# Kernel tuning notes

Measured on AMD Instinct MI355X. Metric: run time of the kernel, lower is better.

Reference implementation:

```python
import jax, jax.numpy as jnp
import numpy as np
from jax import lax

# Mamba hyperparams (mamba_ssm defaults for d_model=768)
D_MODEL = 768
N_LAYER = 8
D_INNER = 2 * D_MODEL          # 1536
D_STATE = 16
DT_RANK = D_MODEL // 16        # 48
D_CONV = 4
BATCH = 4
SEQLEN = 1024


def _ln(x, w, b):
    mu = jnp.mean(x, axis=-1, keepdims=True)
    var = jnp.mean(jnp.square(x - mu), axis=-1, keepdims=True)
    return (x - mu) * lax.rsqrt(var + 1e-5) * w + b


def _silu(x):
    return x * jax.nn.sigmoid(x)


def _mamba_mixer(h, in_proj, conv_w, conv_b, x_proj, dt_w, dt_b, A_log, Dv, out_proj):
    # h: [B, L, d_model]
    xz = jnp.einsum('bld,ed->ble', h, in_proj)          # [B, L, 2*d_inner]
    xm, z = jnp.split(xz, 2, axis=-1)
    # causal depthwise conv1d over time
    xc = lax.conv_general_dilated(
        xm.transpose(0, 2, 1), conv_w, (1,), [(D_CONV - 1, 0)],
        feature_group_count=D_INNER)                    # [B, d_inner, L]
    u = _silu((xc + conv_b[None, :, None]).transpose(0, 2, 1))  # [B, L, d_inner]
    dbc = jnp.einsum('bld,ed->ble', u, x_proj)          # [B, L, dt_rank+2*d_state]
    dt = jax.nn.softplus(jnp.einsum('blr,dr->bld', dbc[..., :DT_RANK], dt_w) + dt_b)
    Bm = dbc[..., DT_RANK:DT_RANK + D_STATE]            # [B, L, d_state]
    Cm = dbc[..., DT_RANK + D_STATE:]                   # [B, L, d_state]
    A = -jnp.exp(A_log)                                 # [d_inner, d_state]

    def step(hstate, inp):
        dt_t, B_t, u_t, C_t = inp                       # [B,d_inner],[B,d_state],[B,d_inner],[B,d_state]
        dA = jnp.exp(dt_t[..., None] * A)               # [B, d_inner, d_state]
        hstate = dA * hstate + (dt_t * u_t)[..., None] * B_t[:, None, :]
        y = jnp.einsum('bds,bs->bd', hstate, C_t)
        return hstate, y

    h0 = jnp.zeros((h.shape[0], D_INNER, D_STATE), h.dtype)
    _, ys = lax.scan(step, h0, (dt.transpose(1, 0, 2), Bm.transpose(1, 0, 2),
                                u.transpose(1, 0, 2), Cm.transpose(1, 0, 2)))
    y = ys.transpose(1, 0, 2) + u * Dv                  # skip connection D*u
    y = y * _silu(z)
    return jnp.einsum('ble,de->bld', y, out_proj)


def setup_inputs() -> dict:
    key = jax.random.key(0)
    ks = jax.random.split(key, 16)
    f32 = jnp.float32
    d = {
        'x': jax.random.normal(ks[0], (BATCH, SEQLEN, D_MODEL), f32),
        'pos': jax.random.normal(ks[1], (BATCH, SEQLEN, D_MODEL), f32),
        'norm_w': jnp.ones((N_LAYER, D_MODEL), f32),
        'norm_b': jnp.zeros((N_LAYER, D_MODEL), f32),
        'in_proj': jax.random.normal(ks[2], (N_LAYER, 2 * D_INNER, D_MODEL), f32) * 0.02,
        'conv_w': jax.random.normal(ks[3], (N_LAYER, D_INNER, 1, D_CONV), f32) * 0.2,
        'conv_b': jnp.zeros((N_LAYER, D_INNER), f32),
        'x_proj': jax.random.normal(ks[4], (N_LAYER, DT_RANK + 2 * D_STATE, D_INNER), f32) * 0.02,
        'dt_w': jax.random.normal(ks[5], (N_LAYER, D_INNER, DT_RANK), f32) * 0.1,
        'dt_b': jax.random.uniform(ks[6], (N_LAYER, D_INNER), f32, -4.0, -2.0),
        'A_log': jnp.broadcast_to(jnp.log(jnp.arange(1, D_STATE + 1, dtype=f32)),
                                  (N_LAYER, D_INNER, D_STATE)).copy(),
        'Dv': jnp.ones((N_LAYER, D_INNER), f32),
        'out_proj': jax.random.normal(ks[7], (N_LAYER, D_MODEL, D_INNER), f32) * 0.02,
        'normf_w': jnp.ones((D_MODEL,), f32),
        'normf_b': jnp.zeros((D_MODEL,), f32),
        'dec_w': jnp.ones((D_MODEL,), f32),
        'dec_b': jnp.zeros((D_MODEL,), f32),
        'return_token_num': 256,
    }
    return d


def reference(x, pos, norm_w, norm_b, in_proj, conv_w, conv_b, x_proj, dt_w, dt_b,
              A_log, Dv, out_proj, normf_w, normf_b, dec_w, dec_b, return_token_num):
    hidden = x + pos
    residual = None
    for l in range(N_LAYER):
        residual = hidden if residual is None else hidden + residual
        h = _ln(residual, norm_w[l], norm_b[l])
        hidden = _mamba_mixer(h, in_proj[l], conv_w[l], conv_b[l], x_proj[l],
                              dt_w[l], dt_b[l], A_log[l], Dv[l], out_proj[l])
    residual = hidden + residual
    hidden = _ln(residual, normf_w, normf_b)
    return _ln(hidden[:, -return_token_num:], dec_w, dec_b)
```

## Files before the change

### kernel.cpp

```cpp
#include <hip/hip_runtime.h>
#include <math.h>

#define D_MODEL 768
#define N_LAYER 8
#define D_INNER 1536
#define D_STATE 16
#define DT_RANK 48
#define D_CONV  4
#define BATCH   4
#define SEQLEN  1024
#define NTOK    (BATCH*SEQLEN)
#define DBC_W   (DT_RANK + 2*D_STATE)
#define NC      64
#define CHUNK_T (SEQLEN/NC)
#define XP_KS   16
#define XP_KSL  (D_INNER/XP_KS)
#define CONV_TCH 16
#define OP_KS   4

typedef __attribute__((ext_vector_type(8))) short short8v;
typedef __attribute__((ext_vector_type(4))) float float4v;

__device__ __forceinline__ void split_bf16(float x, short& hi, short& lo) {
  unsigned u = __float_as_uint(x);
  unsigned r = (u + 0x7fffu + ((u >> 16) & 1u)) >> 16;
  hi = (short)r;
  float fhi = __uint_as_float(r << 16);
  float xl = x - fhi;
  unsigned u2 = __float_as_uint(xl);
  unsigned r2 = (u2 + 0x7fffu + ((u2 >> 16) & 1u)) >> 16;
  lo = (short)r2;
}

__device__ __forceinline__ void gload16(const short* g, short* l) {
  __builtin_amdgcn_global_load_lds(
      (const __attribute__((address_space(1))) void*)g,
      (__attribute__((address_space(3))) void*)l, 16, 0, 0);
}

__global__ __launch_bounds__(256) void split_kernel(
    const float* __restrict__ src, short* __restrict__ hi,
    short* __restrict__ lo, int n4) {
  int stride = gridDim.x * 256;
  for (int i = blockIdx.x * 256 + threadIdx.x; i < n4; i += stride) {
    float4 v = ((const float4*)src)[i];
    short4 h, g;
    split_bf16(v.x, h.x, g.x);
    split_bf16(v.y, h.y, g.y);
    split_bf16(v.z, h.z, g.z);
    split_bf16(v.w, h.w, g.w);
    ((short4*)hi)[i] = h;
    ((short4*)lo)[i] = g;
  }
}

__global__ __launch_bounds__(256) void ln_kernel(
    const float* __restrict__ x, const float* __restrict__ pos,
    float* __restrict__ resid, const float* __restrict__ hy,
    short* __restrict__ hh_hi, short* __restrict__ hh_lo,
    const float* __restrict__ w, const float* __restrict__ b, int first) {
  int row = blockIdx.x;
  int tid = threadIdx.x;
  int base = row * D_MODEL;
  __shared__ float red[256];
  __shared__ float s_mu, s_rs;
  float v[3];
#pragma unroll
  for (int i = 0; i < 3; ++i) {
    int c = tid + i * 256;
    float r;
    if (first) r = x[base + c] + pos[base + c];
    else       r = resid[base + c] + hy[base + c];
    resid[base + c] = r;
    v[i] = r;
  }
  float s = v[0] + v[1] + v[2];
  red[tid] = s; __syncthreads();
  for (int off = 128; off > 0; off >>= 1) {
    if (tid < off) red[tid] += red[tid + off];
    __syncthreads();
  }
  if (tid == 0) s_mu = red[0] / D_MODEL;
  __syncthreads();
  float mu = s_mu;
  float q = 0.f;
#pragma unroll
  for (int i = 0; i < 3; ++i) { float d = v[i] - mu; q += d * d; }
  __syncthreads();
  red[tid] = q; __syncthreads();
  for (int off = 128; off > 0; off >>= 1) {
    if (tid < off) red[tid] += red[tid + off];
    __syncthreads();
  }
  if (tid == 0) s_rs = rsqrtf(red[0] / D_MODEL + 1e-5f);
  __syncthreads();
  float rs = s_rs;
#pragma unroll
  for (int i = 0; i < 3; ++i) {
    int c = tid + i * 256;
    float val = (v[i] - mu) * rs * w[c] + b[c];
    short hv, lv; split_bf16(val, hv, lv);
    hh_hi[base + c] = hv;
    hh_lo[base + c] = lv;
  }
}

__global__ __launch_bounds__(256) void gemm_bf16x3(
    const short* __restrict__ Ahi, const short* __restrict__ Alo, int lda,
    const short* __restrict__ Bhi, const short* __restrict__ Blo, int ldb,
    float* __restrict__ C, int M, int N, int K) {
  const int BK = 32;
  __shared__ short Ash[128][32];
  __shared__ short Asl[128][32];
  __shared__ short Bsh[128][32];
  __shared__ short Bsl[128][32];
  int brow = blockIdx.y * 128;
  int bcol = blockIdx.x * 128;
  int ksl = K / gridDim.z;
  int kbeg = blockIdx.z * ksl;
  int kend = kbeg + ksl;
  float* Cw = C + (size_t)blockIdx.z * M * N;
  int tid = threadIdx.x;
  int wv = tid >> 6, l = tid & 63;
  int wr = (wv >> 1) * 64;
  int wc = (wv & 1) * 64;
  int lrow = l & 15;
  int rslot = ((l >> 4) ^ ((l >> 1) & 3)) * 8;
  int lr = l >> 2;
  int lp = l & 3;
  float4v zero = {0.f, 0.f, 0.f, 0.f};
  float4v acc[4][4];
#pragma unroll
  for (int m = 0; m < 4; ++m)
#pragma unroll
    for (int n = 0; n < 4; ++n) acc[m][n] = zero;

  for (int k0 = kbeg; k0 < kend; k0 += BK) {
#pragma unroll
    for (int half = 0; half < 2; ++half) {
      int row = wv * 32 + half * 16 + lr;
      int s = lp ^ ((row >> 1) & 3);
      int ldsrow = wv * 32 + half * 16;
      size_t ao = (size_t)(brow + row) * lda + k0 + s * 8;
      size_t bo = (size_t)(bcol + row) * ldb + k0 + s * 8;
      gload16(Ahi + ao, &Ash[ldsrow][0]);
      gload16(Alo + ao, &Asl[ldsrow][0]);
      gload16(Bhi + bo, &Bsh[ldsrow][0]);
      gload16(Blo + bo, &Bsl[ldsrow][0]);
    }
    __syncthreads();
    short8v ah[4], al[4];
#pragma unroll
    for (int m = 0; m < 4; ++m) {
      int R = wr + m * 16 + lrow;
      ah[m] = *(const short8v*)&Ash[R][rslot];
      al[m] = *(const short8v*)&Asl[R][rslot];
    }
#pragma unroll
    for (int n = 0; n < 4; ++n) {
      int R = wc + n * 16 + lrow;
      short8v bh = *(const short8v*)&Bsh[R][rslot];
      short8v bl = *(const short8v*)&Bsl[R][rslot];
#pragma unroll
      for (int m = 0; m < 4; ++m) {
        acc[m][n] = __builtin_amdgcn_mfma_f32_16x16x32_bf16(ah[m], bh, acc[m][n], 0, 0, 0);
        acc[m][n] = __builtin_amdgcn_mfma_f32_16x16x32_bf16(ah[m], bl, acc[m][n], 0, 0, 0);
        acc[m][n] = __builtin_amdgcn_mfma_f32_16x16x32_bf16(al[m], bh, acc[m][n], 0, 0, 0);
      }
    }
    __syncthreads();
  }
  int drow = (l >> 4) * 4, dcol = l & 15;
#pragma unroll
  for (int m = 0; m < 4; ++m)
#pragma unroll
    for (int n = 0; n < 4; ++n)
#pragma unroll
      for (int j = 0; j < 4; ++j)
        Cw[(size_t)(brow + wr + m * 16 + drow + j) * N + bcol + wc + n * 16 + dcol] =
            acc[m][n][j];
}

__global__ __launch_bounds__(256) void reduce_out_kernel(
    const float* __restrict__ part, float* __restrict__ out, int n4) {
  int i = blockIdx.x * 256 + threadIdx.x;
  if (i >= n4) return;
  float4 s = ((const float4*)part)[i];
#pragma unroll
  for (int k = 1; k < OP_KS; ++k) {
    float4 v = ((const float4*)(part + (size_t)k * NTOK * D_MODEL))[i];
    s.x += v.x; s.y += v.y; s.z += v.z; s.w += v.w;
  }
  ((float4*)out)[i] = s;
}

__global__ __launch_bounds__(256) void gemm_abt(
    const float* __restrict__ A, int lda, const float* __restrict__ B, int ldb,
    float* __restrict__ C, int M, int N, int K) {
  const int BM = 128, BN = 128, BK = 16;
  __shared__ __align__(16) float As[BK][BM + 4];
  __shared__ __align__(16) float Bs[BK][BN + 4];
  int brow = blockIdx.y * BM;
  int bcol = blockIdx.x * BN;
  int tid = threadIdx.x;
  int tr = (tid / 16) * 4;
  int tc = (tid % 16) * 4;
  float acc[2][2][4][4] = {};
  for (int k0 = 0; k0 < K; k0 += BK) {
#pragma unroll
    for (int it = 0; it < 2; ++it) {
      int idx = tid + it * 256;
      int r  = idx >> 2;
      int cq = (idx & 3) * 4;
      float4 a = *(const float4*)&A[(size_t)(brow + r) * lda + k0 + cq];
      As[cq + 0][r] = a.x; As[cq + 1][r] = a.y;
      As[cq + 2][r] = a.z; As[cq + 3][r] = a.w;
      float4 b = *(const float4*)&B[(size_t)(bcol + r) * ldb + k0 + cq];
      Bs[cq + 0][r] = b.x; Bs[cq + 1][r] = b.y;
      Bs[cq + 2][r] = b.z; Bs[cq + 3][r] = b.w;
    }
    __syncthreads();
#pragma unroll
    for (int kk = 0; kk < BK; ++kk) {
      float4 a0 = *(const float4*)&As[kk][tr];
      float4 a1 = *(const float4*)&As[kk][tr + 64];
      float4 b0 = *(const float4*)&Bs[kk][tc];
      float4 b1 = *(const float4*)&Bs[kk][tc + 64];
      float ar[2][4] = {{a0.x, a0.y, a0.z, a0.w}, {a1.x, a1.y, a1.z, a1.w}};
      float br[2][4] = {{b0.x, b0.y, b0.z, b0.w}, {b1.x, b1.y, b1.z, b1.w}};
#pragma unroll
      for (int rh = 0; rh < 2; ++rh)
#pragma unroll
        for (int ch = 0; ch < 2; ++ch)
#pragma unroll
          for (int i = 0; i < 4; ++i)
#pragma unroll
            for (int j = 0; j < 4; ++j)
              acc[rh][ch][i][j] += ar[rh][i] * br[ch][j];
    }
    __syncthreads();
  }
#pragma unroll
  for (int rh = 0; rh < 2; ++rh)
#pragma unroll
    for (int i = 0; i < 4; ++i) {
      int row = brow + tr + rh * 64 + i;
#pragma unroll
      for (int ch = 0; ch < 2; ++ch) {
        float4 o = make_float4(acc[rh][ch][i][0], acc[rh][ch][i][1],
                               acc[rh][ch][i][2], acc[rh][ch][i][3]);
        *(float4*)&C[(size_t)row * N + bcol + tc + ch * 64] = o;
      }
    }
}

__global__ __launch_bounds__(256) void xproj_gemm(
    const float* __restrict__ u, const float* __restrict__ xp,
    float* __restrict__ part) {
  const int BM = 64, BK = 32;
  __shared__ __align__(16) float As[BK][BM + 4];
  __shared__ float Bs[BK][DBC_W + 1];
  int brow = blockIdx.x * BM;
  int kbase = blockIdx.y * XP_KSL;
  int tid = threadIdx.x;
  int tr = (tid / 16) * 4;
  int tc = (tid % 16) * 5;
  float acc[4][5] = {};
  for (int k0 = kbase; k0 < kbase + XP_KSL; k0 += BK) {
#pragma unroll
    for (int it = 0; it < 2; ++it) {
      int lin = tid + it * 256;
      int r  = lin >> 3;
      int kq = (lin & 7) * 4;
      float4 a = *(const float4*)&u[(size_t)(brow + r) * D_INNER + k0 + kq];
      As[kq + 0][r] = a.x; As[kq + 1][r] = a.y;
      As[kq + 2][r] = a.z; As[kq + 3][r] = a.w;
    }
#pragma unroll
    for (int it = 0; it < 3; ++it) {
      int lin = tid + it * 256;
      if (lin < 640) {
        int e  = lin >> 3;
        int kq = (lin & 7) * 4;
        float4 bv = *(const float4*)&xp[(size_t)e * D_INNER + k0 + kq];
        Bs[kq + 0][e] = bv.x; Bs[kq + 1][e] = bv.y;
        Bs[kq + 2][e] = bv.z; Bs[kq + 3][e] = bv.w;
      }
    }
    __syncthreads();
#pragma unroll
    for (int kk = 0; kk < BK; ++kk) {
      float4 av = *(const float4*)&As[kk][tr];
      float ar[4] = {av.x, av.y, av.z, av.w};
      float br[5];
#pragma unroll
      for (int j = 0; j < 5; ++j) br[j] = Bs[kk][tc + j];
#pragma unroll
      for (int i = 0; i < 4; ++i)
#pragma unroll
        for (int j = 0; j < 5; ++j) acc[i][j] += ar[i] * br[j];
    }
    __syncthreads();
  }
  float* dst = part + (size_t)blockIdx.y * NTOK * DBC_W;
#pragma unroll
  for (int i = 0; i < 4; ++i)
#pragma unroll
    for (int j = 0; j < 5; ++j)
      dst[(size_t)(brow + tr + i) * DBC_W + tc + j] = acc[i][j];
}

__global__ __launch_bounds__(256) void reduce_dbc_kernel(
    const float* __restrict__ part, float* __restrict__ dbc, int n4) {
  int i = blockIdx.x * 256 + threadIdx.x;
  if (i >= n4) return;
  float4 s = ((const float4*)part)[i];
#pragma unroll
  for (int k = 1; k < XP_KS; ++k) {
    float4 v = ((const float4*)(part + (size_t)k * NTOK * DBC_W))[i];
    s.x += v.x; s.y += v.y; s.z += v.z; s.w += v.w;
  }
  ((float4*)dbc)[i] = s;
}

__global__ __launch_bounds__(256) void conv_silu_kernel(
    const float* __restrict__ xz, const float* __restrict__ cw,
    const float* __restrict__ cb, float* __restrict__ u) {
  int idx = blockIdx.x * 256 + threadIdx.x;
  const int NTC = SEQLEN / CONV_TCH;
  if (idx >= BATCH * NTC * D_INNER) return;
  int c  = idx % D_INNER;
  int tc = (idx / D_INNER) % NTC;
  int b  = idx / (D_INNER * NTC);
  int t0 = tc * CONV_TCH;
  float w0 = cw[c * 4 + 0], w1 = cw[c * 4 + 1];
  float w2 = cw[c * 4 + 2], w3 = cw[c * 4 + 3];
  float bias = cb[c];
  const float* base = xz + (size_t)b * SEQLEN * (2 * D_INNER) + c;
  float xm3 = 0.f, xm2 = 0.f, xm1 = 0.f;
  if (t0 > 0) {
    xm3 = base[(size_t)(t0 - 3) * (2 * D_INNER)];
    xm2 = base[(size_t)(t0 - 2) * (2 * D_INNER)];
    xm1 = base[(size_t)(t0 - 1) * (2 * D_INNER)];
  }
  float* ub = u + (size_t)(b * SEQLEN + t0) * D_INNER + c;
#pragma unroll
  for (int i = 0; i < CONV_TCH; ++i) {
    float xt = base[(size_t)(t0 + i) * (2 * D_INNER)];
    float acc = bias + xm3 * w0 + xm2 * w1 + xm1 * w2 + xt * w3;
    float sig = 1.f / (1.f + __expf(-acc));
    ub[(size_t)i * D_INNER] = acc * sig;
    xm3 = xm2; xm2 = xm1; xm1 = xt;
  }
}

__device__ __forceinline__ float softplusf(float a) {
  return (a > 20.f) ? a : log1pf(__expf(a));
}

__global__ __launch_bounds__(256) void scan_chunk1(
    const float* __restrict__ dty, const float* __restrict__ u,
    const float* __restrict__ dbc, const float* __restrict__ A_log,
    const float* __restrict__ dtb,
    float* __restrict__ S, float* __restrict__ dtsum) {
  int blk = blockIdx.x;
  int bcq = (blk * 256) / D_INNER;
  int d = blk * 256 - bcq * D_INNER + threadIdx.x;
  int c = bcq & (NC - 1);
  int b = bcq / NC;
  float A[D_STATE];
#pragma unroll
  for (int s = 0; s < D_STATE; ++s) A[s] = -__expf(A_log[d * D_STATE + s]);
  float bias = dtb[d];
  float h[D_STATE];
#pragma unroll
  for (int s = 0; s < D_STATE; ++s) h[s] = 0.f;
  float dts = 0.f;
  int t0 = c * CHUNK_T;
  for (int t = t0; t < t0 + CHUNK_T; ++t) {
    size_t rowb = (size_t)b * SEQLEN + t;
    const float* bc = dbc + rowb * DBC_W;
    float dtv = softplusf(dty[rowb * D_INNER + d] + bias);
    float uv  = u[rowb * D_INNER + d];
    float dtu = dtv * uv;
    dts += dtv;
#pragma unroll
    for (int s = 0; s < D_STATE; ++s) {
      float da = __expf(dtv * A[s]);
      h[s] = da * h[s] + dtu * bc[DT_RANK + s];
    }
  }
  size_t base = (((size_t)b * NC + c) * D_STATE) * D_INNER + d;
#pragma unroll
  for (int s = 0; s < D_STATE; ++s) S[base + (size_t)s * D_INNER] = h[s];
  dtsum[((size_t)b * NC + c) * D_INNER + d] = dts;
}

__global__ __launch_bounds__(256) void scan_combine(
    float* __restrict__ S, const float* __restrict__ dtsum,
    const float* __restrict__ A_log) {
  int g = blockIdx.x * 256 + threadIdx.x;
  if (g >= BATCH * D_STATE * D_INNER) return;
  int d = g % D_INNER;
  int s = (g / D_INNER) % D_STATE;
  int b = g / (D_INNER * D_STATE);
  float A = -__expf(A_log[d * D_STATE + s]);
  float h = 0.f;
  for (int c = 0; c < NC; ++c) {
    size_t off = (((size_t)b * NC + c) * D_STATE + s) * D_INNER + d;
    float dts = dtsum[((size_t)b * NC + c) * D_INNER + d];
    float Sv = S[off];
    S[off] = h;
    h = __expf(dts * A) * h + Sv;
  }
}

__global__ __launch_bounds__(256) void scan_chunk2(
    const float* __restrict__ dty, const float* __restrict__ u,
    const float* __restrict__ dbc, const float* __restrict__ xz,
    const float* __restrict__ A_log, const float* __restrict__ dtb,
    const float* __restrict__ Dv, const float* __restrict__ hin,
    short* __restrict__ y_hi, short* __restrict__ y_lo) {
  int blk = blockIdx.x;
  int bcq = (blk * 256) / D_INNER;
  int d = blk * 256 - bcq * D_INNER + threadIdx.x;
  int c = bcq & (NC - 1);
  int b = bcq / NC;
  float A[D_STATE];
#pragma unroll
  for (int s = 0; s < D_STATE; ++s) A[s] = -__expf(A_log[d * D_STATE + s]);
  float bias = dtb[d];
  float Dval = Dv[d];
  float h[D_STATE];
  size_t hbase = (((size_t)b * NC + c) * D_STATE) * D_INNER + d;
#pragma unroll
  for (int s = 0; s < D_STATE; ++s) h[s] = hin[hbase + (size_t)s * D_INNER];
  int t0 = c * CHUNK_T;
  for (int t = t0; t < t0 + CHUNK_T; ++t) {
    size_t rowb = (size_t)b * SEQLEN + t;
    const float* bc = dbc + rowb * DBC_W;
    float dtv = softplusf(dty[rowb * D_INNER + d] + bias);
    float uv  = u[rowb * D_INNER + d];
    float dtu = dtv * uv;
    float yv = 0.f;
#pragma unroll
    for (int s = 0; s < D_STATE; ++s) {
      float da = __expf(dtv * A[s]);
      h[s] = da * h[s] + dtu * bc[DT_RANK + s];
      yv += h[s] * bc[DT_RANK + D_STATE + s];
    }
    float zv = xz[rowb * (2 * D_INNER) + D_INNER + d];
    float sig = 1.f / (1.f + __expf(-zv));
    float yo = (yv + uv * Dval) * (zv * sig);
    short hv, lv; split_bf16(yo, hv, lv);
    y_hi[rowb * D_INNER + d] = hv;
    y_lo[rowb * D_INNER + d] = lv;
  }
}

__global__ __launch_bounds__(256) void final_kernel(
    const float* __restrict__ hy, const float* __restrict__ resid,
    const float* __restrict__ fw, const float* __restrict__ fb,
    const float* __restrict__ dw, const float* __restrict__ db,
    float* __restrict__ out, int rtn) {
  int rowo = blockIdx.x;
  int b = rowo / rtn;
  int t = SEQLEN - rtn + (rowo % rtn);
  int tid = threadIdx.x;
  size_t base = ((size_t)b * SEQLEN + t) * D_MODEL;
  __shared__ float red[256];
  __shared__ float s_mu1, s_rs1, s_mu2, s_rs2;
  float v[3];
#pragma unroll
  for (int i = 0; i < 3; ++i) {
    int c = tid + i * 256;
    v[i] = hy[base + c] + resid[base + c];
  }
  red[tid] = v[0] + v[1] + v[2]; __syncthreads();
  for (int off = 128; off > 0; off >>= 1) {
    if (tid < off) red[tid] += red[tid + off];
    __syncthreads();
  }
  if (tid == 0) s_mu1 = red[0] / D_MODEL;
  __syncthreads();
  float mu = s_mu1, q = 0.f;
#pragma unroll
  for (int i = 0; i < 3; ++i) { float dd = v[i] - mu; q += dd * dd; }
  __syncthreads();
  red[tid] = q; __syncthreads();
  for (int off = 128; off > 0; off >>= 1) {
    if (tid < off) red[tid] += red[tid + off];
    __syncthreads();
  }
  if (tid == 0) s_rs1 = rsqrtf(red[0] / D_MODEL + 1e-5f);
  __syncthreads();
  float rs = s_rs1;
#pragma unroll
  for (int i = 0; i < 3; ++i) {
    int c = tid + i * 256;
    v[i] = (v[i] - mu) * rs * fw[c] + fb[c];
  }
  __syncthreads();
  red[tid] = v[0] + v[1] + v[2]; __syncthreads();
  for (int off = 128; off > 0; off >>= 1) {
    if (tid < off) red[tid] += red[tid + off];
    __syncthreads();
  }
  if (tid == 0) s_mu2 = red[0] / D_MODEL;
  __syncthreads();
  mu = s_mu2; q = 0.f;
#pragma unroll
  for (int i = 0; i < 3; ++i) { float dd = v[i] - mu; q += dd * dd; }
  __syncthreads();
  red[tid] = q; __syncthreads();
  for (int off = 128; off > 0; off >>= 1) {
    if (tid < off) red[tid] += red[tid + off];
    __syncthreads();
  }
  if (tid == 0) s_rs2 = rsqrtf(red[0] / D_MODEL + 1e-5f);
  __syncthreads();
  rs = s_rs2;
#pragma unroll
  for (int i = 0; i < 3; ++i) {
    int c = tid + i * 256;
    out[(size_t)rowo * D_MODEL + c] = (v[i] - mu) * rs * dw[c] + db[c];
  }
}

extern "C" void kernel_launch(void* const* d_in, const int* in_sizes, int n_in,
                              void* d_out, int out_size, void* d_ws, size_t ws_size,
                              hipStream_t stream) {
  const float* x       = (const float*)d_in[0];
  const float* pos     = (const float*)d_in[1];
  const float* norm_w  = (const float*)d_in[2];
  const float* norm_b  = (const float*)d_in[3];
  const float* in_proj = (const float*)d_in[4];
  const float* conv_w  = (const float*)d_in[5];
  const float* conv_b  = (const float*)d_in[6];
  const float* x_proj  = (const float*)d_in[7];
  const float* dt_w    = (const float*)d_in[8];
  const float* dt_b    = (const float*)d_in[9];
  const float* A_log   = (const float*)d_in[10];
  const float* Dv      = (const float*)d_in[11];
  const float* out_proj= (const float*)d_in[12];
  const float* normf_w = (const float*)d_in[13];
  const float* normf_b = (const float*)d_in[14];
  const float* dec_w   = (const float*)d_in[15];
  const float* dec_b   = (const float*)d_in[16];
  int rtn = out_size / (BATCH * D_MODEL);

  float* ws    = (float*)d_ws;
  float* resid = ws;
  float* hy    = resid + (size_t)NTOK * D_MODEL;
  float* xz    = hy    + (size_t)NTOK * D_MODEL;
  float* u     = xz    + (size_t)NTOK * 2 * D_INNER;
  float* dbc   = u     + (size_t)NTOK * D_INNER;
  float* dty   = dbc   + (size_t)NTOK * DBC_W;
  float* Sbuf  = dty   + (size_t)NTOK * D_INNER;
  float* dtsum = Sbuf  + (size_t)BATCH * NC * D_STATE * D_INNER;
  float* dbcp  = dtsum + (size_t)BATCH * NC * D_INNER;
  short* hh_hi = (short*)(dbcp + (size_t)XP_KS * NTOK * DBC_W);
  short* hh_lo = hh_hi + (size_t)NTOK * D_MODEL;
  short* y_hi  = hh_lo + (size_t)NTOK * D_MODEL;
  short* y_lo  = y_hi  + (size_t)NTOK * D_INNER;
  short* wbh   = y_lo  + (size_t)NTOK * D_INNER;
  short* wbl   = wbh   + (size_t)2 * D_INNER * D_MODEL;
  float* opart = xz;

  for (int l = 0; l < N_LAYER; ++l) {
    split_kernel<<<1024, 256, 0, stream>>>(
        in_proj + (size_t)l * 2 * D_INNER * D_MODEL, wbh, wbl,
        2 * D_INNER * D_MODEL / 4);

    ln_kernel<<<NTOK, 256, 0, stream>>>(x, pos, resid, hy, hh_hi, hh_lo,
        norm_w + l * D_MODEL, norm_b + l * D_MODEL, l == 0);

    dim3 g1(2 * D_INNER / 128, NTOK / 128, 1);
    gemm_bf16x3<<<g1, 256, 0, stream>>>(hh_hi, hh_lo, D_MODEL,
        wbh, wbl, D_MODEL, xz, NTOK, 2 * D_INNER, D_MODEL);

    int convtot = BATCH * (SEQLEN / CONV_TCH) * D_INNER;
    conv_silu_kernel<<<(convtot + 255) / 256, 256, 0, stream>>>(
        xz, conv_w + (size_t)l * D_INNER * D_CONV, conv_b + l * D_INNER, u);

    dim3 gxp(NTOK / 64, XP_KS);
    xproj_gemm<<<gxp, 256, 0, stream>>>(
        u, x_proj + (size_t)l * DBC_W * D_INNER, dbcp);
    reduce_dbc_kernel<<<(NTOK * DBC_W / 4 + 255) / 256, 256, 0, stream>>>(
        dbcp, dbc, NTOK * DBC_W / 4);

    dim3 gdt(D_INNER / 128, NTOK / 128);
    gemm_abt<<<gdt, 256, 0, stream>>>(dbc, DBC_W,
        dt_w + (size_t)l * D_INNER * DT_RANK, DT_RANK, dty,
        NTOK, D_INNER, DT_RANK);

    const float* Al = A_log + (size_t)l * D_INNER * D_STATE;
    const float* dtbl = dt_b + (size_t)l * D_INNER;
    int tot1 = BATCH * NC * D_INNER;
    scan_chunk1<<<tot1 / 256, 256, 0, stream>>>(
        dty, u, dbc, Al, dtbl, Sbuf, dtsum);
    scan_combine<<<(BATCH * D_STATE * D_INNER + 255) / 256, 256, 0, stream>>>(
        Sbuf, dtsum, Al);
    scan_chunk2<<<tot1 / 256, 256, 0, stream>>>(
        dty, u, dbc, xz, Al, dtbl, Dv + l * D_INNER, Sbuf, y_hi, y_lo);

    split_kernel<<<1024, 256, 0, stream>>>(
        out_proj + (size_t)l * D_MODEL * D_INNER, wbh, wbl,
        D_MODEL * D_INNER / 4);

    dim3 g2(D_MODEL / 128, NTOK / 128, OP_KS);
    gemm_bf16x3<<<g2, 256, 0, stream>>>(y_hi, y_lo, D_INNER,
        wbh, wbl, D_INNER, opart, NTOK, D_MODEL, D_INNER);
    reduce_out_kernel<<<(NTOK * D_MODEL / 4 + 255) / 256, 256, 0, stream>>>(
        opart, hy, NTOK * D_MODEL / 4);
  }

  final_kernel<<<BATCH * rtn, 256, 0, stream>>>(
      hy, resid, normf_w, normf_b, dec_w, dec_b, (float*)d_out, rtn);
}
```

Before: 2.365 ms.

## Fuse dt projection into scan, fold out-proj reduction into LN, hoist weight splits

Result: faster. 2.139 ms (-9.6%).

```diff
diff --git a/kernel.cpp b/kernel.cpp
--- a/kernel.cpp
+++ b/kernel.cpp
@@ -56,7 +56,7 @@
 
 __global__ __launch_bounds__(256) void ln_kernel(
     const float* __restrict__ x, const float* __restrict__ pos,
-    float* __restrict__ resid, const float* __restrict__ hy,
+    float* __restrict__ resid, const float* __restrict__ opart,
     short* __restrict__ hh_hi, short* __restrict__ hh_lo,
     const float* __restrict__ w, const float* __restrict__ b, int first) {
   int row = blockIdx.x;
@@ -69,8 +69,15 @@
   for (int i = 0; i < 3; ++i) {
     int c = tid + i * 256;
     float r;
-    if (first) r = x[base + c] + pos[base + c];
-    else       r = resid[base + c] + hy[base + c];
+    if (first) {
+      r = x[base + c] + pos[base + c];
+    } else {
+      float hysum = opart[base + c];
+#pragma unroll
+      for (int k = 1; k < OP_KS; ++k)
+        hysum += opart[(size_t)k * NTOK * D_MODEL + base + c];
+      r = resid[base + c] + hysum;
+    }
     resid[base + c] = r;
     v[i] = r;
   }
@@ -181,79 +188,6 @@
             acc[m][n][j];
 }
 
-__global__ __launch_bounds__(256) void reduce_out_kernel(
-    const float* __restrict__ part, float* __restrict__ out, int n4) {
-  int i = blockIdx.x * 256 + threadIdx.x;
-  if (i >= n4) return;
-  float4 s = ((const float4*)part)[i];
-#pragma unroll
-  for (int k = 1; k < OP_KS; ++k) {
-    float4 v = ((const float4*)(part + (size_t)k * NTOK * D_MODEL))[i];
-    s.x += v.x; s.y += v.y; s.z += v.z; s.w += v.w;
-  }
-  ((float4*)out)[i] = s;
-}
-
-__global__ __launch_bounds__(256) void gemm_abt(
-    const float* __restrict__ A, int lda, const float* __restrict__ B, int ldb,
-    float* __restrict__ C, int M, int N, int K) {
-  const int BM = 128, BN = 128, BK = 16;
-  __shared__ __align__(16) float As[BK][BM + 4];
-  __shared__ __align__(16) float Bs[BK][BN + 4];
-  int brow = blockIdx.y * BM;
-  int bcol = blockIdx.x * BN;
-  int tid = threadIdx.x;
-  int tr = (tid / 16) * 4;
-  int tc = (tid % 16) * 4;
-  float acc[2][2][4][4] = {};
-  for (int k0 = 0; k0 < K; k0 += BK) {
-#pragma unroll
-    for (int it = 0; it < 2; ++it) {
-      int idx = tid + it * 256;
-      int r  = idx >> 2;
-      int cq = (idx & 3) * 4;
-      float4 a = *(const float4*)&A[(size_t)(brow + r) * lda + k0 + cq];
-      As[cq + 0][r] = a.x; As[cq + 1][r] = a.y;
-      As[cq + 2][r] = a.z; As[cq + 3][r] = a.w;
-      float4 b = *(const float4*)&B[(size_t)(bcol + r) * ldb + k0 + cq];
-      Bs[cq + 0][r] = b.x; Bs[cq + 1][r] = b.y;
-      Bs[cq + 2][r] = b.z; Bs[cq + 3][r] = b.w;
-    }
-    __syncthreads();
-#pragma unroll
-    for (int kk = 0; kk < BK; ++kk) {
-      float4 a0 = *(const float4*)&As[kk][tr];
-      float4 a1 = *(const float4*)&As[kk][tr + 64];
-      float4 b0 = *(const float4*)&Bs[kk][tc];
-      float4 b1 = *(const float4*)&Bs[kk][tc + 64];
-      float ar[2][4] = {{a0.x, a0.y, a0.z, a0.w}, {a1.x, a1.y, a1.z, a1.w}};
-      float br[2][4] = {{b0.x, b0.y, b0.z, b0.w}, {b1.x, b1.y, b1.z, b1.w}};
-#pragma unroll
-      for (int rh = 0; rh < 2; ++rh)
-#pragma unroll
-        for (int ch = 0; ch < 2; ++ch)
-#pragma unroll
-          for (int i = 0; i < 4; ++i)
-#pragma unroll
-            for (int j = 0; j < 4; ++j)
-              acc[rh][ch][i][j] += ar[rh][i] * br[ch][j];
-    }
-    __syncthreads();
-  }
-#pragma unroll
-  for (int rh = 0; rh < 2; ++rh)
-#pragma unroll
-    for (int i = 0; i < 4; ++i) {
-      int row = brow + tr + rh * 64 + i;
-#pragma unroll
-      for (int ch = 0; ch < 2; ++ch) {
-        float4 o = make_float4(acc[rh][ch][i][0], acc[rh][ch][i][1],
-                               acc[rh][ch][i][2], acc[rh][ch][i][3]);
-        *(float4*)&C[(size_t)row * N + bcol + tc + ch * 64] = o;
-      }
-    }
-}
-
 __global__ __launch_bounds__(256) void xproj_gemm(
     const float* __restrict__ u, const float* __restrict__ xp,
     float* __restrict__ part) {
@@ -359,9 +293,9 @@
 }
 
 __global__ __launch_bounds__(256) void scan_chunk1(
-    const float* __restrict__ dty, const float* __restrict__ u,
+    float* __restrict__ dty, const float* __restrict__ u,
     const float* __restrict__ dbc, const float* __restrict__ A_log,
-    const float* __restrict__ dtb,
+    const float* __restrict__ dtw, const float* __restrict__ dtb,
     float* __restrict__ S, float* __restrict__ dtsum) {
   int blk = blockIdx.x;
   int bcq = (blk * 256) / D_INNER;
@@ -371,6 +305,16 @@
   float A[D_STATE];
 #pragma unroll
   for (int s = 0; s < D_STATE; ++s) A[s] = -__expf(A_log[d * D_STATE + s]);
+  float w[DT_RANK];
+  {
+    const float4* w4 = (const float4*)(dtw + (size_t)d * DT_RANK);
+#pragma unroll
+    for (int j = 0; j < DT_RANK / 4; ++j) {
+      float4 v = w4[j];
+      w[j * 4 + 0] = v.x; w[j * 4 + 1] = v.y;
+      w[j * 4 + 2] = v.z; w[j * 4 + 3] = v.w;
+    }
+  }
   float bias = dtb[d];
   float h[D_STATE];
 #pragma unroll
@@ -380,7 +324,11 @@
   for (int t = t0; t < t0 + CHUNK_T; ++t) {
     size_t rowb = (size_t)b * SEQLEN + t;
     const float* bc = dbc + rowb * DBC_W;
-    float dtv = softplusf(dty[rowb * D_INNER + d] + bias);
+    float raw = bias;
+#pragma unroll
+    for (int k = 0; k < DT_RANK; ++k) raw += bc[k] * w[k];
+    float dtv = softplusf(raw);
+    dty[rowb * D_INNER + d] = dtv;
     float uv  = u[rowb * D_INNER + d];
     float dtu = dtv * uv;
     dts += dtv;
@@ -418,7 +366,7 @@
 __global__ __launch_bounds__(256) void scan_chunk2(
     const float* __restrict__ dty, const float* __restrict__ u,
     const float* __restrict__ dbc, const float* __restrict__ xz,
-    const float* __restrict__ A_log, const float* __restrict__ dtb,
+    const float* __restrict__ A_log,
     const float* __restrict__ Dv, const float* __restrict__ hin,
     short* __restrict__ y_hi, short* __restrict__ y_lo) {
   int blk = blockIdx.x;
@@ -429,7 +377,6 @@
   float A[D_STATE];
 #pragma unroll
   for (int s = 0; s < D_STATE; ++s) A[s] = -__expf(A_log[d * D_STATE + s]);
-  float bias = dtb[d];
   float Dval = Dv[d];
   float h[D_STATE];
   size_t hbase = (((size_t)b * NC + c) * D_STATE) * D_INNER + d;
@@ -439,7 +386,7 @@
   for (int t = t0; t < t0 + CHUNK_T; ++t) {
     size_t rowb = (size_t)b * SEQLEN + t;
     const float* bc = dbc + rowb * DBC_W;
-    float dtv = softplusf(dty[rowb * D_INNER + d] + bias);
+    float dtv = dty[rowb * D_INNER + d];
     float uv  = u[rowb * D_INNER + d];
     float dtu = dtv * uv;
     float yv = 0.f;
@@ -459,7 +406,7 @@
 }
 
 __global__ __launch_bounds__(256) void final_kernel(
-    const float* __restrict__ hy, const float* __restrict__ resid,
+    const float* __restrict__ opart, const float* __restrict__ resid,
     const float* __restrict__ fw, const float* __restrict__ fb,
     const float* __restrict__ dw, const float* __restrict__ db,
     float* __restrict__ out, int rtn) {
@@ -474,7 +421,11 @@
 #pragma unroll
   for (int i = 0; i < 3; ++i) {
     int c = tid + i * 256;
-    v[i] = hy[base + c] + resid[base + c];
+    float hysum = opart[base + c];
+#pragma unroll
+    for (int k = 1; k < OP_KS; ++k)
+      hysum += opart[(size_t)k * NTOK * D_MODEL + base + c];
+    v[i] = hysum + resid[base + c];
   }
   red[tid] = v[0] + v[1] + v[2]; __syncthreads();
   for (int off = 128; off > 0; off >>= 1) {
@@ -549,35 +500,40 @@
   const float* dec_b   = (const float*)d_in[16];
   int rtn = out_size / (BATCH * D_MODEL);
 
+  const size_t WI = (size_t)2 * D_INNER * D_MODEL;
+  const size_t WO = (size_t)D_MODEL * D_INNER;
+
   float* ws    = (float*)d_ws;
   float* resid = ws;
-  float* hy    = resid + (size_t)NTOK * D_MODEL;
-  float* xz    = hy    + (size_t)NTOK * D_MODEL;
+  float* xz    = resid + (size_t)NTOK * D_MODEL;
   float* u     = xz    + (size_t)NTOK * 2 * D_INNER;
   float* dbc   = u     + (size_t)NTOK * D_INNER;
   float* dty   = dbc   + (size_t)NTOK * DBC_W;
   float* Sbuf  = dty   + (size_t)NTOK * D_INNER;
   float* dtsum = Sbuf  + (size_t)BATCH * NC * D_STATE * D_INNER;
-  float* dbcp  = dtsum + (size_t)BATCH * NC * D_INNER;
-  short* hh_hi = (short*)(dbcp + (size_t)XP_KS * NTOK * DBC_W);
+  float* dbcp  = Sbuf;
+  short* hh_hi = (short*)(dtsum + (size_t)BATCH * NC * D_INNER);
   short* hh_lo = hh_hi + (size_t)NTOK * D_MODEL;
   short* y_hi  = hh_lo + (size_t)NTOK * D_MODEL;
   short* y_lo  = y_hi  + (size_t)NTOK * D_INNER;
-  short* wbh   = y_lo  + (size_t)NTOK * D_INNER;
-  short* wbl   = wbh   + (size_t)2 * D_INNER * D_MODEL;
+  short* wIh   = y_lo  + (size_t)NTOK * D_INNER;
+  short* wIl   = wIh + N_LAYER * WI;
+  short* wOh   = wIl + N_LAYER * WI;
+  short* wOl   = wOh + N_LAYER * WO;
   float* opart = xz;
 
+  split_kernel<<<2048, 256, 0, stream>>>(in_proj, wIh, wIl,
+                                         (int)(N_LAYER * WI / 4));
+  split_kernel<<<2048, 256, 0, stream>>>(out_proj, wOh, wOl,
+                                         (int)(N_LAYER * WO / 4));
+
   for (int l = 0; l < N_LAYER; ++l) {
-    split_kernel<<<1024, 256, 0, stream>>>(
-        in_proj + (size_t)l * 2 * D_INNER * D_MODEL, wbh, wbl,
-        2 * D_INNER * D_MODEL / 4);
-
-    ln_kernel<<<NTOK, 256, 0, stream>>>(x, pos, resid, hy, hh_hi, hh_lo,
+    ln_kernel<<<NTOK, 256, 0, stream>>>(x, pos, resid, opart, hh_hi, hh_lo,
         norm_w + l * D_MODEL, norm_b + l * D_MODEL, l == 0);
 
     dim3 g1(2 * D_INNER / 128, NTOK / 128, 1);
     gemm_bf16x3<<<g1, 256, 0, stream>>>(hh_hi, hh_lo, D_MODEL,
-        wbh, wbl, D_MODEL, xz, NTOK, 2 * D_INNER, D_MODEL);
+        wIh + l * WI, wIl + l * WI, D_MODEL, xz, NTOK, 2 * D_INNER, D_MODEL);
 
     int convtot = BATCH * (SEQLEN / CONV_TCH) * D_INNER;
     conv_silu_kernel<<<(convtot + 255) / 256, 256, 0, stream>>>(
@@ -589,32 +545,21 @@
     reduce_dbc_kernel<<<(NTOK * DBC_W / 4 + 255) / 256, 256, 0, stream>>>(
         dbcp, dbc, NTOK * DBC_W / 4);
 
-    dim3 gdt(D_INNER / 128, NTOK / 128);
-    gemm_abt<<<gdt, 256, 0, stream>>>(dbc, DBC_W,
-        dt_w + (size_t)l * D_INNER * DT_RANK, DT_RANK, dty,
-        NTOK, D_INNER, DT_RANK);
-
     const float* Al = A_log + (size_t)l * D_INNER * D_STATE;
-    const float* dtbl = dt_b + (size_t)l * D_INNER;
     int tot1 = BATCH * NC * D_INNER;
     scan_chunk1<<<tot1 / 256, 256, 0, stream>>>(
-        dty, u, dbc, Al, dtbl, Sbuf, dtsum);
+        dty, u, dbc, Al, dt_w + (size_t)l * D_INNER * DT_RANK,
+        dt_b + (size_t)l * D_INNER, Sbuf, dtsum);
     scan_combine<<<(BATCH * D_STATE * D_INNER + 255) / 256, 256, 0, stream>>>(
         Sbuf, dtsum, Al);
     scan_chunk2<<<tot1 / 256, 256, 0, stream>>>(
-        dty, u, dbc, xz, Al, dtbl, Dv + l * D_INNER, Sbuf, y_hi, y_lo);
-
-    split_kernel<<<1024, 256, 0, stream>>>(
-        out_proj + (size_t)l * D_MODEL * D_INNER, wbh, wbl,
-        D_MODEL * D_INNER / 4);
+        dty, u, dbc, xz, Al, Dv + l * D_INNER, Sbuf, y_hi, y_lo);
 
     dim3 g2(D_MODEL / 128, NTOK / 128, OP_KS);
     gemm_bf16x3<<<g2, 256, 0, stream>>>(y_hi, y_lo, D_INNER,
-        wbh, wbl, D_INNER, opart, NTOK, D_MODEL, D_INNER);
-    reduce_out_kernel<<<(NTOK * D_MODEL / 4 + 255) / 256, 256, 0, stream>>>(
-        opart, hy, NTOK * D_MODEL / 4);
+        wOh + l * WO, wOl + l * WO, D_INNER, opart, NTOK, D_MODEL, D_INNER);
   }
 
   final_kernel<<<BATCH * rtn, 256, 0, stream>>>(
-      hy, resid, normf_w, normf_b, dec_w, dec_b, (float*)d_out, rtn);
-}
+      opart, resid, normf_w, normf_b, dec_w, dec_b, (float*)d_out, rtn);
+}
```
